# Kernel tuning notes

Measured on AMD Instinct MI355X. Metric: run time of the kernel, lower is better.

The kernel has to match this reference:

```python
import jax, jax.numpy as jnp
import numpy as np

N_NODES = 50000
N_EDGES = 1_600_000
IN_DIM = 128
HID = 32
HEADS = 4
NEG_SLOPE = 0.2


def setup_inputs() -> dict:
    key = jax.random.key(0)
    ks = jax.random.split(key, 6)
    h = jax.random.normal(ks[0], (N_NODES, IN_DIM), dtype=jnp.float32)
    src = jax.random.randint(ks[1], (N_EDGES,), 0, N_NODES, dtype=jnp.int32)
    dst = jax.random.randint(ks[2], (N_EDGES,), 0, N_NODES, dtype=jnp.int32)
    s = 1.0 / np.sqrt(IN_DIM)  # ~ Linear default init scale
    Wq = (jax.random.normal(ks[3], (HEADS, IN_DIM, HID), dtype=jnp.float32) * s)
    Wk = (jax.random.normal(ks[4], (HEADS, IN_DIM, HID), dtype=jnp.float32) * s)
    Wv = (jax.random.normal(ks[5], (HEADS, IN_DIM, HID), dtype=jnp.float32) * s)
    return {"h": h, "src": src, "dst": dst, "Wq": Wq, "Wk": Wk, "Wv": Wv}


def _gat_forward(h, src, dst, Wq, Wk, Wv):
    n = h.shape[0]
    # per-head projections: [H, N, D]
    q = jnp.einsum('ni,hio->hno', h, Wq)
    k = jnp.einsum('ni,hio->hno', h, Wk)
    v = jnp.einsum('ni,hio->hno', h, Wv)
    # edge scores: e = leaky_relu(<q_src, k_dst>)  -> [H, E]
    e = jax.nn.leaky_relu(jnp.einsum('hed,hed->he', q[:, src], k[:, dst]),
                          negative_slope=NEG_SLOPE)
    # segment softmax over incoming edges of each dst node
    seg_max = jax.vmap(lambda x: jax.ops.segment_max(x, dst, num_segments=n))(e)
    seg_max = jax.lax.stop_gradient(jnp.where(jnp.isfinite(seg_max), seg_max, 0.0))
    ex = jnp.exp(e - seg_max[:, dst])                       # [H, E]
    denom = jax.vmap(lambda x: jax.ops.segment_sum(x, dst, num_segments=n))(ex)
    alpha = ex / jnp.maximum(denom, 1e-9)[:, dst]           # [H, E]
    # weighted scatter-sum of source values into dst nodes: [H, N, D]
    msg = alpha[..., None] * v[:, src]
    out = jax.vmap(lambda m: jax.ops.segment_sum(m, dst, num_segments=n))(msg)
    # concat heads along feature dim -> [N, H*D]
    return out.transpose(1, 0, 2).reshape(n, HEADS * HID)


def reference(h, src, dst, Wq, Wk, Wv):
    return _gat_forward(h, src, dst, Wq, Wk, Wv)
```

## Files before the change

### kernel.cpp

```cpp
#include <hip/hip_runtime.h>
#include <hip/hip_fp16.h>

#define IN_DIM 128
#define HID 32
#define HEADS 4
#define OUTC (HEADS*HID)
#define NEG_SLOPE 0.2f
#define BSH 4
#define BN 16
#define BCAP 768
#define NBMAX 3200
#define NCOLS 384
#define WPB 192
#define NP 25
#define PSH 11
#define PCAP 72704
#define PBLK 18
#define OSTRIDE 392

typedef _Float16 f16x8 __attribute__((ext_vector_type(8)));
typedef float    f32x4 __attribute__((ext_vector_type(4)));

__device__ __forceinline__ unsigned short f2h(float f) {
    return __half_as_ushort(__float2half_rn(f));
}
__device__ __forceinline__ float2 h2f2(unsigned u) {
    __half2 h = *reinterpret_cast<__half2*>(&u);
    return __half22float2(h);
}
__device__ __forceinline__ float qdot2(const uint2& w, const float4& kd) {
    float2 a = h2f2(w.x);
    float2 b = h2f2(w.y);
    return a.x * kd.x + a.y * kd.y + b.x * kd.z + b.y * kd.w;
}
__device__ __forceinline__ void vacc2(const uint2& w, float e, float4& acc) {
    float2 a = h2f2(w.x);
    float2 b = h2f2(w.y);
    acc.x = fmaf(e, a.x, acc.x);
    acc.y = fmaf(e, a.y, acc.y);
    acc.z = fmaf(e, b.x, acc.z);
    acc.w = fmaf(e, b.y, acc.w);
}

__global__ __launch_bounds__(256) void kA_prep_part(
    const float* __restrict__ Wq, const float* __restrict__ Wk,
    const float* __restrict__ Wv, unsigned short* __restrict__ Wt,
    int* __restrict__ pcount,
    const int* __restrict__ src, const int* __restrict__ dst,
    unsigned* __restrict__ ppairs, int ne)
{
    const int tid = threadIdx.x;

    if ((int)blockIdx.x < WPB) {
        int idx = blockIdx.x * 256 + tid;
        if (idx >= NCOLS * IN_DIM) return;
        int c = idx >> 7, k = idx & 127;
        int sel = c >> 7;
        int cc  = c & 127;
        int head = cc >> 5, dcol = cc & 31;
        const float* W = (sel == 0) ? Wk : (sel == 1) ? Wq : Wv;
        Wt[idx] = f2h(W[(size_t)head * IN_DIM * HID + (size_t)k * HID + dcol]);
        return;
    }

    __shared__ int hist[4 * 32];
    __shared__ int base[4 * 32];
    const int bblk = blockIdx.x - WPB;
    const int wid  = tid >> 6;

    if (tid < 128) hist[tid] = 0;
    __syncthreads();

    const int ne4 = ne >> 2;
    const int4* s4 = (const int4*)src;
    const int4* d4 = (const int4*)dst;

    int4 sv[4], dv[4];
    int loc[16], pk[16];
    bool val[4];
#pragma unroll
    for (int k2 = 0; k2 < 4; ++k2) {
        int idx = bblk * 1024 + k2 * 256 + tid;
        val[k2] = idx < ne4;
        if (val[k2]) { sv[k2] = s4[idx]; dv[k2] = d4[idx]; }
        else { sv[k2] = make_int4(0,0,0,0); dv[k2] = make_int4(0,0,0,0); }
    }
#pragma unroll
    for (int k2 = 0; k2 < 4; ++k2) {
        int dd[4] = { dv[k2].x, dv[k2].y, dv[k2].z, dv[k2].w };
#pragma unroll
        for (int j = 0; j < 4; ++j) {
            int p = dd[j] >> PSH;
            pk[k2*4+j]  = p;
            loc[k2*4+j] = val[k2] ? atomicAdd(&hist[wid * 32 + p], 1) : 0;
        }
    }
    __syncthreads();
    if (tid < 128)
        base[tid] = hist[tid] ? atomicAdd(&pcount[tid & 31], hist[tid]) : 0;
    __syncthreads();
#pragma unroll
    for (int k2 = 0; k2 < 4; ++k2) {
        if (!val[k2]) continue;
        int ss[4] = { sv[k2].x, sv[k2].y, sv[k2].z, sv[k2].w };
        int dd[4] = { dv[k2].x, dv[k2].y, dv[k2].z, dv[k2].w };
#pragma unroll
        for (int j = 0; j < 4; ++j) {
            int p   = pk[k2*4+j];
            int pos = base[wid * 32 + p] + loc[k2*4+j];
            if (pos >= 0 && pos < PCAP)
                ppairs[(size_t)p * PCAP + pos] =
                    ((unsigned)ss[j] << 16) | (unsigned)dd[j];
        }
    }
    if (bblk == 0 && tid == 0) {
        for (int e = ne4 * 4; e < ne; ++e) {
            int p   = dst[e] >> PSH;
            int pos = atomicAdd(&pcount[p], 1);
            if (pos >= 0 && pos < PCAP)
                ppairs[(size_t)p * PCAP + pos] =
                    ((unsigned)src[e] << 16) | (unsigned)dst[e];
        }
    }
}

__global__ __launch_bounds__(256) void kB_bin_proj(
    const unsigned* __restrict__ ppairs, const int* __restrict__ pcount,
    int* __restrict__ gcount, unsigned* __restrict__ pairs,
    const float* __restrict__ h, const unsigned short* __restrict__ Wt,
    unsigned short* __restrict__ K, unsigned short* __restrict__ Qa,
    unsigned short* __restrict__ Va,
    int p2blk, int n)
{
    __shared__ __align__(16) char smem_raw[32 * OSTRIDE * 2];
    const int tid = threadIdx.x;

    if ((int)blockIdx.x < p2blk) {
        int* hist = (int*)smem_raw;
        int* base = hist + 128;
        const int p = blockIdx.x / PBLK;
        const int c = blockIdx.x % PBLK;

        int mp = pcount[p]; if (mp > PCAP) mp = PCAP;
        const int i0 = c * 4096;
        if (i0 >= mp) return;
        const int iend = min(i0 + 4096, mp);

        if (tid < 128) hist[tid] = 0;
        __syncthreads();

        const unsigned* pp = ppairs + (size_t)p * PCAP;
        unsigned rec[16];
        int loc[16], lb[16];
#pragma unroll
        for (int k = 0; k < 16; ++k) {
            int i = i0 + k * 256 + tid;
            if (i < iend) {
                unsigned r = pp[i];
                rec[k] = r;
                int b = ((r & 0xFFFFu) >> BSH) & 127;
                lb[k]  = b;
                loc[k] = atomicAdd(&hist[b], 1);
            } else {
                rec[k] = 0; lb[k] = -1; loc[k] = 0;
            }
        }
        __syncthreads();
        if (tid < 128)
            base[tid] = hist[tid] ? atomicAdd(&gcount[p * 128 + tid], hist[tid]) : 0;
        __syncthreads();
#pragma unroll
        for (int k = 0; k < 16; ++k) {
            if (lb[k] < 0) continue;
            unsigned r = rec[k];
            int gb  = p * 128 + lb[k];
            int pos = base[lb[k]] + loc[k];
            if (pos < BCAP)
                pairs[(size_t)gb * BCAP + pos] =
                    ((r >> 16) << BSH) | (r & (BN - 1));
        }
        return;
    }

    unsigned short* hsm = (unsigned short*)smem_raw;
    const int row0 = (blockIdx.x - p2blk) * 32;

    for (int idx = tid; idx < 32 * 32; idx += 256) {
        int r  = idx >> 5;
        int c4 = idx & 31;
        int gr = row0 + r;
        float4 hv = (gr < n) ? ((const float4*)h)[(size_t)gr * 32 + c4]
                             : make_float4(0.f, 0.f, 0.f, 0.f);
        int sc = (c4 * 4) ^ ((r & 7) << 3);
        __half2 p01 = __floats2half2_rn(hv.x, hv.y);
        __half2 p23 = __floats2half2_rn(hv.z, hv.w);
        uint2 u;
        u.x = *(unsigned*)&p01;
        u.y = *(unsigned*)&p23;
        *(uint2*)&hsm[r * IN_DIM + sc] = u;
    }
    __syncthreads();

    const int w = tid >> 6;
    const int l = tid & 63;
    const int l15 = l & 15;
    const int kg  = l >> 4;
    const _Float16* Wt16 = (const _Float16*)Wt;

    f32x4 acc[2][6];
#pragma unroll
    for (int rt = 0; rt < 2; ++rt)
#pragma unroll
        for (int ct = 0; ct < 6; ++ct) acc[rt][ct] = (f32x4){0.f, 0.f, 0.f, 0.f};

#pragma unroll
    for (int s = 0; s < 4; ++s) {
        int scol = (s * 32 + kg * 8) ^ ((l & 7) << 3);
        f16x8 a0 = *(const f16x8*)&hsm[l15 * IN_DIM + scol];
        f16x8 a1 = *(const f16x8*)&hsm[(l15 + 16) * IN_DIM + scol];
#pragma unroll
        for (int ct = 0; ct < 6; ++ct) {
            int c = w * 96 + ct * 16 + l15;
            f16x8 b = *(const f16x8*)&Wt16[(size_t)c * IN_DIM + s * 32 + kg * 8];
            acc[0][ct] = __builtin_amdgcn_mfma_f32_16x16x32_f16(a0, b, acc[0][ct], 0, 0, 0);
            acc[1][ct] = __builtin_amdgcn_mfma_f32_16x16x32_f16(a1, b, acc[1][ct], 0, 0, 0);
        }
    }
    __syncthreads();

    unsigned short* osm = (unsigned short*)smem_raw;
#pragma unroll
    for (int rt = 0; rt < 2; ++rt) {
#pragma unroll
        for (int ct = 0; ct < 6; ++ct) {
            int cD = w * 96 + ct * 16 + l15;
#pragma unroll
            for (int r = 0; r < 4; ++r) {
                int rowl = rt * 16 + kg * 4 + r;
                osm[rowl * OSTRIDE + cD] = f2h(acc[rt][ct][r]);
            }
        }
    }
    __syncthreads();

    for (int c = tid; c < 32 * 96; c += 256) {
        int row  = c / 96;
        int col4 = c - row * 96;
        int node = row0 + row;
        if (node >= n) continue;
        uint2 v = *(const uint2*)&osm[row * OSTRIDE + col4 * 4];
        int colbase = col4 * 4;
        if (colbase < 128)
            *(uint2*)&K [(size_t)node * OUTC + colbase] = v;
        else if (colbase < 256)
            *(uint2*)&Qa[(size_t)node * OUTC + (colbase - 128)] = v;
        else
            *(uint2*)&Va[(size_t)node * OUTC + (colbase - 256)] = v;
    }
}

__global__ __launch_bounds__(256) void gat_bucket(
    const unsigned* __restrict__ pairs, const int* __restrict__ gcount,
    const uint2* __restrict__ Q2, const uint2* __restrict__ V2,
    const ushort4* __restrict__ K4,
    float* __restrict__ out, int n, int nbuck)
{
    __shared__ unsigned short sl[BCAP];
    __shared__ float exls[BCAP * 4];
    __shared__ int cl[BN], cur[BN], off[BN + 1];

    const int b = blockIdx.x;
    if (b >= nbuck) return;
    const int tid = threadIdx.x;

    if (tid < BN) cl[tid] = 0;
    __syncthreads();

    int m = gcount[b]; if (m > BCAP) m = BCAP;
    const unsigned* pb = pairs + (size_t)b * BCAP;

    for (int i = tid; i < m; i += 256) atomicAdd(&cl[pb[i] & (BN - 1)], 1);
    __syncthreads();
    if (tid == 0) {
        int a = 0;
#pragma unroll
        for (int i = 0; i < BN; ++i) { off[i] = a; cur[i] = a; a += cl[i]; }
        off[BN] = a;
    }
    __syncthreads();
    for (int i = tid; i < m; i += 256) {
        unsigned p = pb[i];
        int pos = atomicAdd(&cur[p & (BN - 1)], 1);
        sl[pos] = (unsigned short)(p >> BSH);
    }
    __syncthreads();

    const int gi   = tid >> 5;
    const int l32  = tid & 31;
    const int hsel = l32 >> 3;
    const bool wr  = (l32 & 7) == 0;

    float dsum[BN / 8];

#pragma unroll
    for (int q = 0; q < BN / 8; ++q) {
        int nl   = q * 8 + gi;
        int node = b * BN + nl;
        float ds = 0.f;
        if (node < n) {
            ushort4 kh = K4[(size_t)node * 32 + l32];
            float2 k01 = h2f2(*(unsigned*)&kh.x);
            float2 k23 = h2f2(*(unsigned*)&kh.z);
            const float4 kd = make_float4(k01.x, k01.y, k23.x, k23.y);

            int j        = off[nl];
            const int je = off[nl + 1];
            for (; j + 3 < je; j += 4) {
                int s0 = sl[j], s1 = sl[j + 1], s2 = sl[j + 2], s3 = sl[j + 3];
                uint2 w0 = Q2[(size_t)s0 * 32 + l32];
                uint2 w1 = Q2[(size_t)s1 * 32 + l32];
                uint2 w2 = Q2[(size_t)s2 * 32 + l32];
                uint2 w3 = Q2[(size_t)s3 * 32 + l32];
                float p0 = qdot2(w0, kd), p1 = qdot2(w1, kd);
                float p2 = qdot2(w2, kd), p3 = qdot2(w3, kd);
#pragma unroll
                for (int o = 1; o < 8; o <<= 1) {
                    p0 += __shfl_xor(p0, o, 8);
                    p1 += __shfl_xor(p1, o, 8);
                    p2 += __shfl_xor(p2, o, 8);
                    p3 += __shfl_xor(p3, o, 8);
                }
                float e0 = __expf(p0 > 0.f ? p0 : NEG_SLOPE * p0);
                float e1 = __expf(p1 > 0.f ? p1 : NEG_SLOPE * p1);
                float e2 = __expf(p2 > 0.f ? p2 : NEG_SLOPE * p2);
                float e3 = __expf(p3 > 0.f ? p3 : NEG_SLOPE * p3);
                ds += (e0 + e1) + (e2 + e3);
                if (wr) {
                    exls[(j    ) * 4 + hsel] = e0;
                    exls[(j + 1) * 4 + hsel] = e1;
                    exls[(j + 2) * 4 + hsel] = e2;
                    exls[(j + 3) * 4 + hsel] = e3;
                }
            }
            for (; j < je; ++j) {
                int s0 = sl[j];
                uint2 w0 = Q2[(size_t)s0 * 32 + l32];
                float p0 = qdot2(w0, kd);
#pragma unroll
                for (int o = 1; o < 8; o <<= 1) p0 += __shfl_xor(p0, o, 8);
                float e0 = __expf(p0 > 0.f ? p0 : NEG_SLOPE * p0);
                ds += e0;
                if (wr) exls[j * 4 + hsel] = e0;
            }
        }
        dsum[q] = ds;
    }
    __syncthreads();

#pragma unroll
    for (int q = 0; q < BN / 8; ++q) {
        int nl   = q * 8 + gi;
        int node = b * BN + nl;
        if (node >= n) continue;

        int j        = off[nl];
        const int je = off[nl + 1];
        float4 acc = make_float4(0.f, 0.f, 0.f, 0.f);

        for (; j + 3 < je; j += 4) {
            int s0 = sl[j], s1 = sl[j + 1], s2 = sl[j + 2], s3 = sl[j + 3];
            uint2 w0 = V2[(size_t)s0 * 32 + l32];
            uint2 w1 = V2[(size_t)s1 * 32 + l32];
            uint2 w2 = V2[(size_t)s2 * 32 + l32];
            uint2 w3 = V2[(size_t)s3 * 32 + l32];
            float e0 = exls[(j    ) * 4 + hsel];
            float e1 = exls[(j + 1) * 4 + hsel];
            float e2 = exls[(j + 2) * 4 + hsel];
            float e3 = exls[(j + 3) * 4 + hsel];
            vacc2(w0, e0, acc); vacc2(w1, e1, acc);
            vacc2(w2, e2, acc); vacc2(w3, e3, acc);
        }
        for (; j < je; ++j) {
            int s0 = sl[j];
            uint2 w0 = V2[(size_t)s0 * 32 + l32];
            float e0 = exls[j * 4 + hsel];
            vacc2(w0, e0, acc);
        }

        float inv = 1.f / fmaxf(dsum[q], 1e-9f);
        float4 o; o.x = acc.x*inv; o.y = acc.y*inv; o.z = acc.z*inv; o.w = acc.w*inv;
        ((float4*)out)[(size_t)node * 32 + l32] = o;
    }
}

extern "C" void kernel_launch(void* const* d_in, const int* in_sizes, int n_in,
                              void* d_out, int out_size, void* d_ws, size_t ws_size,
                              hipStream_t stream) {
    const float* h   = (const float*)d_in[0];
    const int*   src = (const int*)d_in[1];
    const int*   dst = (const int*)d_in[2];
    const float* Wq  = (const float*)d_in[3];
    const float* Wk  = (const float*)d_in[4];
    const float* Wv  = (const float*)d_in[5];
    float* out = (float*)d_out;

    const int n     = in_sizes[0] / IN_DIM;
    const int ne    = in_sizes[1];
    const int nbuck = (n + BN - 1) >> BSH;

    unsigned short* K      = (unsigned short*)d_ws;
    unsigned short* Qa     = K  + (size_t)n * OUTC;
    unsigned short* Va     = Qa + (size_t)n * OUTC;
    int*            gcount = (int*)(Va + (size_t)n * OUTC);
    int*            pcount = gcount + NBMAX;
    unsigned*       ppairs = (unsigned*)(pcount + 64);
    unsigned*       pairs  = ppairs + (size_t)NP * PCAP;
    unsigned short* Wt     = (unsigned short*)(pairs + (size_t)NBMAX * BCAP);

    hipMemsetAsync(gcount, 0, (NBMAX + 64) * sizeof(int), stream);

    int ne4    = ne >> 2;
    int binblk = (ne4 + 1023) / 1024;
    kA_prep_part<<<WPB + binblk, 256, 0, stream>>>(
        Wq, Wk, Wv, Wt, pcount, src, dst, ppairs, ne);

    int p2blk   = NP * PBLK;
    int projblk = (n + 31) / 32;
    kB_bin_proj<<<p2blk + projblk, 256, 0, stream>>>(
        ppairs, pcount, gcount, pairs, h, Wt, K, Qa, Va, p2blk, n);

    gat_bucket<<<nbuck, 256, 0, stream>>>(pairs, gcount, (const uint2*)Qa,
                                          (const uint2*)Va, (const ushort4*)K,
                                          out, n, nbuck);
}
```

Before: 201.5 us.

## Split projection across both partition passes and fold memset into weight prep

The weight transpose/convert step becomes its own small kernel, which also zeroes the bucket counters, so the separate memset call goes away. Half of the node projection blocks now run alongside the first edge-partition pass and the other half alongside the second binning pass, so both launches mix compute-heavy and scatter-heavy blocks. The first-pass histogram also drops from per-wavefront copies to a single shared 32-entry histogram. The cost is one more kernel launch and more contention on the shared-memory atomics in the first pass.

```diff
diff --git a/kernel.cpp b/kernel.cpp
--- a/kernel.cpp
+++ b/kernel.cpp
@@ -42,148 +42,13 @@
     acc.w = fmaf(e, b.y, acc.w);
 }
 
-__global__ __launch_bounds__(256) void kA_prep_part(
-    const float* __restrict__ Wq, const float* __restrict__ Wk,
-    const float* __restrict__ Wv, unsigned short* __restrict__ Wt,
-    int* __restrict__ pcount,
-    const int* __restrict__ src, const int* __restrict__ dst,
-    unsigned* __restrict__ ppairs, int ne)
-{
-    const int tid = threadIdx.x;
-
-    if ((int)blockIdx.x < WPB) {
-        int idx = blockIdx.x * 256 + tid;
-        if (idx >= NCOLS * IN_DIM) return;
-        int c = idx >> 7, k = idx & 127;
-        int sel = c >> 7;
-        int cc  = c & 127;
-        int head = cc >> 5, dcol = cc & 31;
-        const float* W = (sel == 0) ? Wk : (sel == 1) ? Wq : Wv;
-        Wt[idx] = f2h(W[(size_t)head * IN_DIM * HID + (size_t)k * HID + dcol]);
-        return;
-    }
-
-    __shared__ int hist[4 * 32];
-    __shared__ int base[4 * 32];
-    const int bblk = blockIdx.x - WPB;
-    const int wid  = tid >> 6;
-
-    if (tid < 128) hist[tid] = 0;
-    __syncthreads();
-
-    const int ne4 = ne >> 2;
-    const int4* s4 = (const int4*)src;
-    const int4* d4 = (const int4*)dst;
-
-    int4 sv[4], dv[4];
-    int loc[16], pk[16];
-    bool val[4];
-#pragma unroll
-    for (int k2 = 0; k2 < 4; ++k2) {
-        int idx = bblk * 1024 + k2 * 256 + tid;
-        val[k2] = idx < ne4;
-        if (val[k2]) { sv[k2] = s4[idx]; dv[k2] = d4[idx]; }
-        else { sv[k2] = make_int4(0,0,0,0); dv[k2] = make_int4(0,0,0,0); }
-    }
-#pragma unroll
-    for (int k2 = 0; k2 < 4; ++k2) {
-        int dd[4] = { dv[k2].x, dv[k2].y, dv[k2].z, dv[k2].w };
-#pragma unroll
-        for (int j = 0; j < 4; ++j) {
-            int p = dd[j] >> PSH;
-            pk[k2*4+j]  = p;
-            loc[k2*4+j] = val[k2] ? atomicAdd(&hist[wid * 32 + p], 1) : 0;
-        }
-    }
-    __syncthreads();
-    if (tid < 128)
-        base[tid] = hist[tid] ? atomicAdd(&pcount[tid & 31], hist[tid]) : 0;
-    __syncthreads();
-#pragma unroll
-    for (int k2 = 0; k2 < 4; ++k2) {
-        if (!val[k2]) continue;
-        int ss[4] = { sv[k2].x, sv[k2].y, sv[k2].z, sv[k2].w };
-        int dd[4] = { dv[k2].x, dv[k2].y, dv[k2].z, dv[k2].w };
-#pragma unroll
-        for (int j = 0; j < 4; ++j) {
-            int p   = pk[k2*4+j];
-            int pos = base[wid * 32 + p] + loc[k2*4+j];
-            if (pos >= 0 && pos < PCAP)
-                ppairs[(size_t)p * PCAP + pos] =
-                    ((unsigned)ss[j] << 16) | (unsigned)dd[j];
-        }
-    }
-    if (bblk == 0 && tid == 0) {
-        for (int e = ne4 * 4; e < ne; ++e) {
-            int p   = dst[e] >> PSH;
-            int pos = atomicAdd(&pcount[p], 1);
-            if (pos >= 0 && pos < PCAP)
-                ppairs[(size_t)p * PCAP + pos] =
-                    ((unsigned)src[e] << 16) | (unsigned)dst[e];
-        }
-    }
-}
-
-__global__ __launch_bounds__(256) void kB_bin_proj(
-    const unsigned* __restrict__ ppairs, const int* __restrict__ pcount,
-    int* __restrict__ gcount, unsigned* __restrict__ pairs,
+__device__ __forceinline__ void proj_body(
+    char* smem_raw, int tid, int row0,
     const float* __restrict__ h, const unsigned short* __restrict__ Wt,
     unsigned short* __restrict__ K, unsigned short* __restrict__ Qa,
-    unsigned short* __restrict__ Va,
-    int p2blk, int n)
+    unsigned short* __restrict__ Va, int n)
 {
-    __shared__ __align__(16) char smem_raw[32 * OSTRIDE * 2];
-    const int tid = threadIdx.x;
-
-    if ((int)blockIdx.x < p2blk) {
-        int* hist = (int*)smem_raw;
-        int* base = hist + 128;
-        const int p = blockIdx.x / PBLK;
-        const int c = blockIdx.x % PBLK;
-
-        int mp = pcount[p]; if (mp > PCAP) mp = PCAP;
-        const int i0 = c * 4096;
-        if (i0 >= mp) return;
-        const int iend = min(i0 + 4096, mp);
-
-        if (tid < 128) hist[tid] = 0;
-        __syncthreads();
-
-        const unsigned* pp = ppairs + (size_t)p * PCAP;
-        unsigned rec[16];
-        int loc[16], lb[16];
-#pragma unroll
-        for (int k = 0; k < 16; ++k) {
-            int i = i0 + k * 256 + tid;
-            if (i < iend) {
-                unsigned r = pp[i];
-                rec[k] = r;
-                int b = ((r & 0xFFFFu) >> BSH) & 127;
-                lb[k]  = b;
-                loc[k] = atomicAdd(&hist[b], 1);
-            } else {
-                rec[k] = 0; lb[k] = -1; loc[k] = 0;
-            }
-        }
-        __syncthreads();
-        if (tid < 128)
-            base[tid] = hist[tid] ? atomicAdd(&gcount[p * 128 + tid], hist[tid]) : 0;
-        __syncthreads();
-#pragma unroll
-        for (int k = 0; k < 16; ++k) {
-            if (lb[k] < 0) continue;
-            unsigned r = rec[k];
-            int gb  = p * 128 + lb[k];
-            int pos = base[lb[k]] + loc[k];
-            if (pos < BCAP)
-                pairs[(size_t)gb * BCAP + pos] =
-                    ((r >> 16) << BSH) | (r & (BN - 1));
-        }
-        return;
-    }
-
     unsigned short* hsm = (unsigned short*)smem_raw;
-    const int row0 = (blockIdx.x - p2blk) * 32;
 
     for (int idx = tid; idx < 32 * 32; idx += 256) {
         int r  = idx >> 5;
@@ -257,6 +122,160 @@
         else
             *(uint2*)&Va[(size_t)node * OUTC + (colbase - 256)] = v;
     }
+}
+
+__global__ __launch_bounds__(256) void w_prep(
+    const float* __restrict__ Wq, const float* __restrict__ Wk,
+    const float* __restrict__ Wv, unsigned short* __restrict__ Wt,
+    int* __restrict__ gcount, int* __restrict__ pcount)
+{
+    int idx = blockIdx.x * 256 + threadIdx.x;
+    if (idx < NBMAX) gcount[idx] = 0;
+    if (idx >= NBMAX && idx < NBMAX + NP) pcount[idx - NBMAX] = 0;
+    if (idx >= NCOLS * IN_DIM) return;
+    int c = idx >> 7, k = idx & 127;
+    int sel = c >> 7;
+    int cc  = c & 127;
+    int head = cc >> 5, dcol = cc & 31;
+    const float* W = (sel == 0) ? Wk : (sel == 1) ? Wq : Wv;
+    Wt[idx] = f2h(W[(size_t)head * IN_DIM * HID + (size_t)k * HID + dcol]);
+}
+
+__global__ __launch_bounds__(256) void part_projA(
+    const int* __restrict__ src, const int* __restrict__ dst,
+    int* __restrict__ pcount, unsigned* __restrict__ ppairs,
+    const float* __restrict__ h, const unsigned short* __restrict__ Wt,
+    unsigned short* __restrict__ K, unsigned short* __restrict__ Qa,
+    unsigned short* __restrict__ Va,
+    int ne, int binblk, int n)
+{
+    __shared__ __align__(16) char smem_raw[32 * OSTRIDE * 2];
+    const int tid = threadIdx.x;
+
+    if ((int)blockIdx.x < binblk) {
+        int* hist = (int*)smem_raw;
+        int* base = hist + 32;
+        const int bblk = blockIdx.x;
+
+        if (tid < 32) hist[tid] = 0;
+        __syncthreads();
+
+        const int ne4 = ne >> 2;
+        const int4* s4 = (const int4*)src;
+        const int4* d4 = (const int4*)dst;
+
+        int4 sv[4], dv[4];
+        int loc[16], pk[16];
+        bool val[4];
+#pragma unroll
+        for (int k2 = 0; k2 < 4; ++k2) {
+            int idx = bblk * 1024 + k2 * 256 + tid;
+            val[k2] = idx < ne4;
+            if (val[k2]) { sv[k2] = s4[idx]; dv[k2] = d4[idx]; }
+            else { sv[k2] = make_int4(0,0,0,0); dv[k2] = make_int4(0,0,0,0); }
+        }
+#pragma unroll
+        for (int k2 = 0; k2 < 4; ++k2) {
+            int dd[4] = { dv[k2].x, dv[k2].y, dv[k2].z, dv[k2].w };
+#pragma unroll
+            for (int j = 0; j < 4; ++j) {
+                int p = dd[j] >> PSH;
+                pk[k2*4+j]  = p;
+                loc[k2*4+j] = val[k2] ? atomicAdd(&hist[p], 1) : 0;
+            }
+        }
+        __syncthreads();
+        if (tid < 32) base[tid] = hist[tid] ? atomicAdd(&pcount[tid], hist[tid]) : 0;
+        __syncthreads();
+#pragma unroll
+        for (int k2 = 0; k2 < 4; ++k2) {
+            if (!val[k2]) continue;
+            int ss[4] = { sv[k2].x, sv[k2].y, sv[k2].z, sv[k2].w };
+            int dd[4] = { dv[k2].x, dv[k2].y, dv[k2].z, dv[k2].w };
+#pragma unroll
+            for (int j = 0; j < 4; ++j) {
+                int p   = pk[k2*4+j];
+                int pos = base[p] + loc[k2*4+j];
+                if (pos < PCAP)
+                    ppairs[(size_t)p * PCAP + pos] =
+                        ((unsigned)ss[j] << 16) | (unsigned)dd[j];
+            }
+        }
+        if (bblk == 0 && tid == 0) {
+            for (int e = ne4 * 4; e < ne; ++e) {
+                int p   = dst[e] >> PSH;
+                int pos = atomicAdd(&pcount[p], 1);
+                if (pos < PCAP)
+                    ppairs[(size_t)p * PCAP + pos] =
+                        ((unsigned)src[e] << 16) | (unsigned)dst[e];
+            }
+        }
+        return;
+    }
+
+    proj_body(smem_raw, tid, (blockIdx.x - binblk) * 32, h, Wt, K, Qa, Va, n);
+}
+
+__global__ __launch_bounds__(256) void pass2_projB(
+    const unsigned* __restrict__ ppairs, const int* __restrict__ pcount,
+    int* __restrict__ gcount, unsigned* __restrict__ pairs,
+    const float* __restrict__ h, const unsigned short* __restrict__ Wt,
+    unsigned short* __restrict__ K, unsigned short* __restrict__ Qa,
+    unsigned short* __restrict__ Va,
+    int p2blk, int rowbase, int n)
+{
+    __shared__ __align__(16) char smem_raw[32 * OSTRIDE * 2];
+    const int tid = threadIdx.x;
+
+    if ((int)blockIdx.x < p2blk) {
+        int* hist = (int*)smem_raw;
+        int* base = hist + 128;
+        const int p = blockIdx.x / PBLK;
+        const int c = blockIdx.x % PBLK;
+
+        int mp = pcount[p]; if (mp > PCAP) mp = PCAP;
+        const int i0 = c * 4096;
+        if (i0 >= mp) return;
+        const int iend = min(i0 + 4096, mp);
+
+        if (tid < 128) hist[tid] = 0;
+        __syncthreads();
+
+        const unsigned* pp = ppairs + (size_t)p * PCAP;
+        unsigned rec[16];
+        int loc[16], lb[16];
+#pragma unroll
+        for (int k = 0; k < 16; ++k) {
+            int i = i0 + k * 256 + tid;
+            if (i < iend) {
+                unsigned r = pp[i];
+                rec[k] = r;
+                int b = ((r & 0xFFFFu) >> BSH) & 127;
+                lb[k]  = b;
+                loc[k] = atomicAdd(&hist[b], 1);
+            } else {
+                rec[k] = 0; lb[k] = -1; loc[k] = 0;
+            }
+        }
+        __syncthreads();
+        if (tid < 128)
+            base[tid] = hist[tid] ? atomicAdd(&gcount[p * 128 + tid], hist[tid]) : 0;
+        __syncthreads();
+#pragma unroll
+        for (int k = 0; k < 16; ++k) {
+            if (lb[k] < 0) continue;
+            unsigned r = rec[k];
+            int gb  = p * 128 + lb[k];
+            int pos = base[lb[k]] + loc[k];
+            if (pos < BCAP)
+                pairs[(size_t)gb * BCAP + pos] =
+                    ((r >> 16) << BSH) | (r & (BN - 1));
+        }
+        return;
+    }
+
+    proj_body(smem_raw, tid, (blockIdx.x - p2blk) * 32 + rowbase,
+              h, Wt, K, Qa, Va, n);
 }
 
 __global__ __launch_bounds__(256) void gat_bucket(
@@ -417,17 +436,21 @@
     unsigned*       pairs  = ppairs + (size_t)NP * PCAP;
     unsigned short* Wt     = (unsigned short*)(pairs + (size_t)NBMAX * BCAP);
 
-    hipMemsetAsync(gcount, 0, (NBMAX + 64) * sizeof(int), stream);
-
-    int ne4    = ne >> 2;
-    int binblk = (ne4 + 1023) / 1024;
-    kA_prep_part<<<WPB + binblk, 256, 0, stream>>>(
-        Wq, Wk, Wv, Wt, pcount, src, dst, ppairs, ne);
-
-    int p2blk   = NP * PBLK;
+    w_prep<<<WPB, 256, 0, stream>>>(Wq, Wk, Wv, Wt, gcount, pcount);
+
+    int ne4     = ne >> 2;
+    int binblk  = (ne4 + 1023) / 1024;
     int projblk = (n + 31) / 32;
-    kB_bin_proj<<<p2blk + projblk, 256, 0, stream>>>(
-        ppairs, pcount, gcount, pairs, h, Wt, K, Qa, Va, p2blk, n);
+    int projA   = (projblk + 1) / 2;
+    int projB   = projblk - projA;
+
+    part_projA<<<binblk + projA, 256, 0, stream>>>(
+        src, dst, pcount, ppairs, h, Wt, K, Qa, Va, ne, binblk, n);
+
+    int p2blk = NP * PBLK;
+    pass2_projB<<<p2blk + projB, 256, 0, stream>>>(
+        ppairs, pcount, gcount, pairs, h, Wt, K, Qa, Va,
+        p2blk, projA * 32, n);
 
     gat_bucket<<<nbuck, 256, 0, stream>>>(pairs, gcount, (const uint2*)Qa,
                                           (const uint2*)Va, (const ushort4*)K,
```

New measurement: 165.0 us (median of 2 runs). 1.22x faster.
